# Optimization experiments

Hardware: AMD Instinct MI355X
Metric: run time of the kernel (lower is better)

The kernel has to match this reference:

```python
import jax, jax.numpy as jnp
import numpy as np

N = 50000
E = 400000
IN_DIM = 128
HID = 128
OUT = 128
HEADS = 8
NEG_SLOPE = 0.2  # PyG GATConv default
BN_EPS = 1e-5


def _gat_conv(x, W, a_src, a_dst, b, src, dst, concat):
    """PyG GATConv (eval): self-loops added by caller. x:[N,F], W:[F,H*C], a_*:[H,C]."""
    H, C = a_src.shape
    xW = (x @ W).reshape(N, H, C)                       # [N,H,C]
    es = jnp.sum(xW * a_src[None], axis=-1)             # [N,H]
    ed = jnp.sum(xW * a_dst[None], axis=-1)             # [N,H]
    e = jax.nn.leaky_relu(es[src] + ed[dst], NEG_SLOPE) # [E,H]
    m = jax.ops.segment_max(e, dst, num_segments=N)     # softmax over incoming edges per dst
    ex = jnp.exp(e - m[dst])
    denom = jax.ops.segment_sum(ex, dst, num_segments=N)
    alpha = ex / denom[dst]                             # [E,H]
    out = jax.ops.segment_sum(xW[src] * alpha[:, :, None], dst, num_segments=N)  # [N,H,C]
    out = out.reshape(N, H * C) if concat else out.mean(axis=1)
    return out + b


def _bn_eval(h, g, be, rm, rv):
    return (h - rm) * jax.lax.rsqrt(rv + BN_EPS) * g + be


def setup_inputs() -> dict:
    key = jax.random.key(0)
    ks = jax.random.split(key, 20)
    C1 = HID // HEADS
    f32 = jnp.float32
    inp = {
        "x": jax.random.normal(ks[0], (N, IN_DIM), dtype=f32),
        "edge_index": jax.random.randint(ks[1], (2, E), 0, N, dtype=jnp.int64),
        # GAT layer 1 (in->hid, 8 heads, concat)
        "W1": jax.random.normal(ks[2], (IN_DIM, HEADS * C1), dtype=f32) * 0.05,
        "a_src1": jax.random.normal(ks[3], (HEADS, C1), dtype=f32) * 0.05,
        "a_dst1": jax.random.normal(ks[4], (HEADS, C1), dtype=f32) * 0.05,
        "b1": jnp.zeros((HEADS * C1,), dtype=f32),
        # GAT layer 2 (hid->hid, 8 heads, concat)
        "W2": jax.random.normal(ks[5], (HID, HEADS * C1), dtype=f32) * 0.05,
        "a_src2": jax.random.normal(ks[6], (HEADS, C1), dtype=f32) * 0.05,
        "a_dst2": jax.random.normal(ks[7], (HEADS, C1), dtype=f32) * 0.05,
        "b2": jnp.zeros((HEADS * C1,), dtype=f32),
        # GAT layer 3 (hid->out, 1 head, no concat)
        "W3": jax.random.normal(ks[8], (HID, OUT), dtype=f32) * 0.05,
        "a_src3": jax.random.normal(ks[9], (1, OUT), dtype=f32) * 0.05,
        "a_dst3": jax.random.normal(ks[10], (1, OUT), dtype=f32) * 0.05,
        "b3": jnp.zeros((OUT,), dtype=f32),
        # residual linears
        "R1w": jax.random.normal(ks[11], (IN_DIM, HID), dtype=f32) * 0.05,
        "R1b": jnp.zeros((HID,), dtype=f32),
        "R2w": jax.random.normal(ks[12], (HID, HID), dtype=f32) * 0.05,
        "R2b": jnp.zeros((HID,), dtype=f32),
        "R3w": jax.random.normal(ks[13], (HID, OUT), dtype=f32) * 0.05,
        "R3b": jnp.zeros((OUT,), dtype=f32),
        # batch norms (eval mode: running stats)
        "g1": jnp.ones((HID,), dtype=f32), "be1": jnp.zeros((HID,), dtype=f32),
        "rm1": jnp.zeros((HID,), dtype=f32), "rv1": jnp.ones((HID,), dtype=f32),
        "g2": jnp.ones((HID,), dtype=f32), "be2": jnp.zeros((HID,), dtype=f32),
        "rm2": jnp.zeros((HID,), dtype=f32), "rv2": jnp.ones((HID,), dtype=f32),
    }
    return inp


def reference(x, edge_index, W1, a_src1, a_dst1, b1, W2, a_src2, a_dst2, b2,
              W3, a_src3, a_dst3, b3, R1w, R1b, R2w, R2b, R3w, R3b,
              g1, be1, rm1, rv1, g2, be2, rm2, rv2):
    # PyG GATConv adds self-loops by default
    loops = jnp.arange(N, dtype=edge_index.dtype)
    src = jnp.concatenate([edge_index[0], loops])
    dst = jnp.concatenate([edge_index[1], loops])

    h = _gat_conv(x, W1, a_src1, a_dst1, b1, src, dst, concat=True) + (x @ R1w + R1b)
    h1 = jax.nn.relu(_bn_eval(h, g1, be1, rm1, rv1))  # dropout identity in eval

    h = _gat_conv(h1, W2, a_src2, a_dst2, b2, src, dst, concat=True) + (h1 @ R2w + R2b)
    h2 = jax.nn.relu(_bn_eval(h, g2, be2, rm2, rv2))

    out = _gat_conv(h2, W3, a_src3, a_dst3, b3, src, dst, concat=False) + (h2 @ R3w + R3b)
    return out
```

## Files before the change

### kernel.cpp

```cpp
#include <hip/hip_runtime.h>
#include <hip/hip_bf16.h>
#include <type_traits>

typedef __hip_bfloat16 bf16;
typedef __hip_bfloat162 bf162;
typedef short v8s __attribute__((ext_vector_type(8)));
typedef float v4f __attribute__((ext_vector_type(4)));

__device__ __forceinline__ float lrelu(float x) { return x > 0.f ? x : 0.2f * x; }
__device__ __forceinline__ float b2f(bf16 v) { return __bfloat162float(v); }

__global__ void k_count(const int* __restrict__ ei, int* __restrict__ cnt, int E) {
    int i = blockIdx.x * 256 + threadIdx.x;
    if (i < E) atomicAdd(&cnt[ei[E + i]], 1);
}

__global__ void k_scan1(const int* __restrict__ cnt, int* __restrict__ ofs,
                        int* __restrict__ bsum, int n) {
    __shared__ int sh[256];
    int t = threadIdx.x;
    int base = blockIdx.x * 1024 + t * 4;
    int v[4]; int s = 0;
#pragma unroll
    for (int i = 0; i < 4; ++i) { v[i] = (base + i < n) ? cnt[base + i] : 0; s += v[i]; }
    sh[t] = s; __syncthreads();
    for (int o = 1; o < 256; o <<= 1) {
        int x = 0; if (t >= o) x = sh[t - o];
        __syncthreads();
        sh[t] += x;
        __syncthreads();
    }
    int excl = sh[t] - s;
#pragma unroll
    for (int i = 0; i < 4; ++i) { if (base + i < n) ofs[base + i] = excl; excl += v[i]; }
    if (t == 255) bsum[blockIdx.x] = sh[255];
}

__global__ void k_scan2(const int* __restrict__ bsum, int* __restrict__ bpre, int nb) {
    int l = threadIdx.x;
    int v = (l < nb) ? bsum[l] : 0;
    int orig = v;
    for (int o = 1; o < 64; o <<= 1) {
        int x = __shfl_up(v, o);
        if (l >= o) v += x;
    }
    if (l < nb) bpre[l] = v - orig;
}

__global__ void k_scan3(int* __restrict__ ofs, int* __restrict__ cur,
                        const int* __restrict__ bpre, int n) {
    int i = blockIdx.x * 256 + threadIdx.x;
    if (i < n) { int v = ofs[i] + bpre[i >> 10]; ofs[i] = v; cur[i] = v; }
}

__global__ void k_fill(const int* __restrict__ ei, int* __restrict__ cur,
                       int* __restrict__ csr, int E) {
    int i = blockIdx.x * 256 + threadIdx.x;
    if (i < E) {
        int d = ei[E + i];
        int pos = atomicAdd(&cur[d], 1);
        csr[pos] = ei[i];
    }
}

__global__ void k_trans(const float* __restrict__ s0, const float* __restrict__ s1,
                        const float* __restrict__ s2, const float* __restrict__ s3,
                        const float* __restrict__ s4, const float* __restrict__ s5,
                        const float* __restrict__ as1, const float* __restrict__ ad1,
                        const float* __restrict__ as2, const float* __restrict__ ad2,
                        const float* __restrict__ as3, const float* __restrict__ ad3,
                        const float* b1, const float* R1b, const float* g1, const float* be1,
                        const float* rm1, const float* rv1,
                        const float* b2, const float* R2b, const float* g2, const float* be2,
                        const float* rm2, const float* rv2,
                        const float* b3, const float* R3b,
                        bf16* __restrict__ wt, float* __restrict__ prm) {
    int b = blockIdx.x;
    int t = threadIdx.x;
    if (b == 6) {
        int c = t;
        if (c < 128) {
            float s1v = g1[c] * rsqrtf(rv1[c] + 1e-5f);
            prm[c]       = b1[c] + R1b[c];
            prm[128 + c] = s1v;
            prm[256 + c] = be1[c] - rm1[c] * s1v;
            float s2v = g2[c] * rsqrtf(rv2[c] + 1e-5f);
            prm[384 + c] = b2[c] + R2b[c];
            prm[512 + c] = s2v;
            prm[640 + c] = be2[c] - rm2[c] * s2v;
            prm[768 + c] = b3[c] + R3b[c];
        }
        return;
    }
    const float* src;
    switch (b) {
        case 0: src = s0; break; case 1: src = s1; break; case 2: src = s2; break;
        case 3: src = s3; break; case 4: src = s4; break; default: src = s5; break;
    }
    bf16* dst = wt + (size_t)b * 18432;
    for (int i = t; i < 16384; i += 256) {
        int k = i >> 7, n = i & 127;
        dst[n * 128 + k] = __float2bfloat16(src[i]);
    }
    if ((b & 1) == 0) {
        int layer = b >> 1;
        if (layer < 2) {
            const float* asr = (layer == 0) ? as1 : as2;
            const float* ads = (layer == 0) ? ad1 : ad2;
            for (int i = t; i < 2048; i += 256) {
                int row = i >> 7, k = i & 127, h = row & 7;
                const float* av = (row < 8) ? asr : ads;
                float s = 0.f;
#pragma unroll
                for (int c = 0; c < 16; ++c) s += src[k * 128 + h * 16 + c] * av[h * 16 + c];
                dst[(128 + row) * 128 + k] = __float2bfloat16(s);
            }
        } else {
            for (int i = t; i < 2048; i += 256) {
                int row = i >> 7, k = i & 127;
                float s = 0.f;
                if (row == 0 || row == 8) {
                    const float* av = (row == 0) ? as3 : ad3;
                    for (int c = 0; c < 128; ++c) s += src[k * 128 + c] * av[c];
                }
                dst[(128 + row) * 128 + k] = __float2bfloat16(s);
            }
        }
    } else {
        for (int i = t; i < 2048; i += 256)
            dst[16384 + i] = __float2bfloat16(0.f);
    }
}

template <typename T>
__global__ void gemm_dual(const T* __restrict__ A,
                          const bf16* __restrict__ BT0, const bf16* __restrict__ BT1,
                          bf16* __restrict__ O0, bf16* __restrict__ O1,
                          float* __restrict__ es, float* __restrict__ ed,
                          int mode, int nrows) {
    __shared__ bf16 Ash[128 * 128];
    __shared__ bf16 Bsh[144 * 128];
    const bf16* BT = (blockIdx.y == 0) ? BT0 : BT1;
    bf16* O = (blockIdx.y == 0) ? O0 : O1;
    const int t = threadIdx.x;
    const int rowbase = blockIdx.x * 128;
    {
        const int r = t >> 1, hf = t & 1;
        int gr = rowbase + r; if (gr >= nrows) gr = nrows - 1;
        if constexpr (std::is_same<T, float>::value) {
            const float4* asrc = (const float4*)(A + (size_t)gr * 128 + hf * 64);
#pragma unroll
            for (int j = 0; j < 8; ++j) {
                float4 u = asrc[2 * j], w = asrc[2 * j + 1];
                union { bf16 h[8]; float4 f; } tmp;
                tmp.h[0] = __float2bfloat16(u.x); tmp.h[1] = __float2bfloat16(u.y);
                tmp.h[2] = __float2bfloat16(u.z); tmp.h[3] = __float2bfloat16(u.w);
                tmp.h[4] = __float2bfloat16(w.x); tmp.h[5] = __float2bfloat16(w.y);
                tmp.h[6] = __float2bfloat16(w.z); tmp.h[7] = __float2bfloat16(w.w);
                int c = hf * 8 + j, cp = c ^ (r & 7);
                *(float4*)(&Ash[r * 128 + cp * 8]) = tmp.f;
            }
        } else {
            const float4* asrc = (const float4*)(A + (size_t)gr * 128 + hf * 64);
#pragma unroll
            for (int j = 0; j < 8; ++j) {
                int c = hf * 8 + j, cp = c ^ (r & 7);
                *(float4*)(&Ash[r * 128 + cp * 8]) = asrc[j];
            }
        }
    }
    for (int s = t; s < 288; s += 256) {
        int r = s >> 1, hf = s & 1;
        const float4* bsrc = (const float4*)(BT + r * 128 + hf * 64);
#pragma unroll
        for (int j = 0; j < 8; ++j) {
            int c = hf * 8 + j, cp = c ^ (r & 7);
            *(float4*)(&Bsh[r * 128 + cp * 8]) = bsrc[j];
        }
    }
    __syncthreads();
    const int wave = t >> 6, lane = t & 63, quad = lane >> 4, l16 = lane & 15;
    v4f acc[2][9];
#pragma unroll
    for (int i = 0; i < 2; ++i)
#pragma unroll
        for (int j = 0; j < 9; ++j) acc[i][j] = (v4f){0.f, 0.f, 0.f, 0.f};
#pragma unroll
    for (int kit = 0; kit < 4; ++kit) {
        v8s afr[2], bfr[9];
#pragma unroll
        for (int rt = 0; rt < 2; ++rt) {
            int row = wave * 32 + rt * 16 + l16;
            int cp = (kit * 4 + quad) ^ (row & 7);
            afr[rt] = *(const v8s*)(&Ash[row * 128 + cp * 8]);
        }
#pragma unroll
        for (int ct = 0; ct < 9; ++ct) {
            int nn = ct * 16 + l16;
            int cp = (kit * 4 + quad) ^ (nn & 7);
            bfr[ct] = *(const v8s*)(&Bsh[nn * 128 + cp * 8]);
        }
#pragma unroll
        for (int rt = 0; rt < 2; ++rt)
#pragma unroll
            for (int ct = 0; ct < 9; ++ct)
                acc[rt][ct] = __builtin_amdgcn_mfma_f32_16x16x32_bf16(afr[rt], bfr[ct], acc[rt][ct], 0, 0, 0);
    }
#pragma unroll
    for (int rt = 0; rt < 2; ++rt)
#pragma unroll
        for (int ct = 0; ct < 8; ++ct)
#pragma unroll
            for (int r = 0; r < 4; ++r) {
                int gr = rowbase + wave * 32 + rt * 16 + quad * 4 + r;
                if (gr < nrows) O[(size_t)gr * 128 + ct * 16 + l16] = __float2bfloat16(acc[rt][ct][r]);
            }
    if (mode != 0 && blockIdx.y == 0) {
#pragma unroll
        for (int rt = 0; rt < 2; ++rt)
#pragma unroll
            for (int r = 0; r < 4; ++r) {
                int gr = rowbase + wave * 32 + rt * 16 + quad * 4 + r;
                if (gr < nrows) {
                    float v = acc[rt][8][r];
                    if (mode == 1) {
                        if (l16 < 8) es[(size_t)gr * 8 + l16] = v;
                        else         ed[(size_t)gr * 8 + (l16 - 8)] = v;
                    } else {
                        if (l16 == 0) es[gr] = v;
                        else if (l16 == 8) ed[gr] = v;
                    }
                }
            }
    }
}

__global__ void k_agg8(const bf16* __restrict__ xW, const float* __restrict__ es8,
                       const float* __restrict__ ed8,
                       const int* __restrict__ ofs, const int* __restrict__ cur,
                       const int* __restrict__ csr,
                       const bf16* __restrict__ rres, const float* __restrict__ prm,
                       bf16* __restrict__ hout, int n) {
    int wave = threadIdx.x >> 6, lane = threadIdx.x & 63;
    int node = blockIdx.x * 4 + wave;
    if (node >= n) return;
    const int g = lane >> 4, l16 = lane & 15;
    const int c0 = l16 * 8;
    const int hc = l16 >> 1;
    const int he = lane & 7;
    float edw = ed8[(size_t)node * 8 + he];
    float wselfh = __expf(lrelu(es8[(size_t)node * 8 + he] + edw));
    float acc[8]; float den = 0.f;
#pragma unroll
    for (int i = 0; i < 8; ++i) acc[i] = 0.f;
    {
        float ws = __shfl(wselfh, hc);
        if (g == 0) {
            v8s xv = *(const v8s*)(xW + (size_t)node * 128 + c0);
            const bf16* xb = (const bf16*)&xv;
            den = ws;
#pragma unroll
            for (int i = 0; i < 8; ++i) acc[i] = ws * b2f(xb[i]);
        }
    }
    int beg = ofs[node], end = cur[node];
    for (int base = beg; base < end; base += 64) {
        int m = end - base; if (m > 64) m = 64;
        int idx = (lane < m) ? csr[base + lane] : node;
        for (int sub = 0; sub * 8 < m; ++sub) {
            int e = sub * 8 + (lane >> 3);
            int sidx = __shfl(idx, e & 63);
            float esv = es8[(size_t)sidx * 8 + he];
            float w = (e < m) ? __expf(lrelu(esv + edw)) : 0.f;
#pragma unroll
            for (int jj = 0; jj < 2; ++jj) {
                int jo = jj * 4 + g;
                int j = sub * 8 + jo;
                int sv = __shfl(idx, j & 63);
                float wj = __shfl(w, jo * 8 + hc);
                v8s xv = *(const v8s*)(xW + (size_t)sv * 128 + c0);
                const bf16* xb = (const bf16*)&xv;
                den += wj;
#pragma unroll
                for (int i = 0; i < 8; ++i) acc[i] += wj * b2f(xb[i]);
            }
        }
    }
    den += __shfl_xor(den, 16); den += __shfl_xor(den, 32);
#pragma unroll
    for (int i = 0; i < 8; ++i) {
        acc[i] += __shfl_xor(acc[i], 16);
        acc[i] += __shfl_xor(acc[i], 32);
    }
    if (g == 0) {
        float inv = 1.f / den;
        v8s rv = *(const v8s*)(rres + (size_t)node * 128 + c0);
        const bf16* rb = (const bf16*)&rv;
        bf16 outv[8];
#pragma unroll
        for (int i = 0; i < 8; ++i) {
            int c = c0 + i;
            float v = acc[i] * inv + prm[c] + b2f(rb[i]);
            v = fmaxf(v * prm[128 + c] + prm[256 + c], 0.f);
            outv[i] = __float2bfloat16(v);
        }
        *(v8s*)(hout + (size_t)node * 128 + c0) = *(v8s*)outv;
    }
}

__global__ void k_agg1(const bf16* __restrict__ xW, const float* __restrict__ es,
                       const float* __restrict__ ed,
                       const int* __restrict__ ofs, const int* __restrict__ cur,
                       const int* __restrict__ csr,
                       const bf16* __restrict__ rres, const float* __restrict__ bias,
                       float* __restrict__ out, int n) {
    int wave = threadIdx.x >> 6, lane = threadIdx.x & 63;
    int node = blockIdx.x * 4 + wave;
    if (node >= n) return;
    const int g = lane >> 4, l16 = lane & 15;
    const int c0 = l16 * 8;
    float edv = ed[node];
    float wself = __expf(lrelu(es[node] + edv));
    float acc[8]; float den = 0.f;
#pragma unroll
    for (int i = 0; i < 8; ++i) acc[i] = 0.f;
    if (g == 0) {
        v8s xv = *(const v8s*)(xW + (size_t)node * 128 + c0);
        const bf16* xb = (const bf16*)&xv;
        den = wself;
#pragma unroll
        for (int i = 0; i < 8; ++i) acc[i] = wself * b2f(xb[i]);
    }
    int beg = ofs[node], end = cur[node];
    for (int base = beg; base < end; base += 64) {
        int m = end - base; if (m > 64) m = 64;
        int idx = (lane < m) ? csr[base + lane] : node;
        float w = (lane < m) ? __expf(lrelu(es[idx] + edv)) : 0.f;
        for (int j = 0; j < m; j += 4) {
            int jl = j + g;
            int sv = __shfl(idx, jl & 63);
            float wj = __shfl(w, jl & 63);
            if (jl >= m) wj = 0.f;
            v8s xv = *(const v8s*)(xW + (size_t)sv * 128 + c0);
            const bf16* xb = (const bf16*)&xv;
            den += wj;
#pragma unroll
            for (int i = 0; i < 8; ++i) acc[i] += wj * b2f(xb[i]);
        }
    }
    den += __shfl_xor(den, 16); den += __shfl_xor(den, 32);
#pragma unroll
    for (int i = 0; i < 8; ++i) {
        acc[i] += __shfl_xor(acc[i], 16);
        acc[i] += __shfl_xor(acc[i], 32);
    }
    if (g == 0) {
        float inv = 1.f / den;
        v8s rv = *(const v8s*)(rres + (size_t)node * 128 + c0);
        const bf16* rb = (const bf16*)&rv;
        float ov[8];
#pragma unroll
        for (int i = 0; i < 8; ++i)
            ov[i] = acc[i] * inv + bias[c0 + i] + b2f(rb[i]);
        float4 o0, o1;
        o0.x = ov[0]; o0.y = ov[1]; o0.z = ov[2]; o0.w = ov[3];
        o1.x = ov[4]; o1.y = ov[5]; o1.z = ov[6]; o1.w = ov[7];
        *(float4*)(out + (size_t)node * 128 + c0) = o0;
        *(float4*)(out + (size_t)node * 128 + c0 + 4) = o1;
    }
}

extern "C" void kernel_launch(void* const* d_in, const int* in_sizes, int n_in,
                              void* d_out, int out_size, void* d_ws, size_t ws_size,
                              hipStream_t stream) {
    const float* x   = (const float*)d_in[0];
    const int*   ei  = (const int*)d_in[1];
    const float* W1  = (const float*)d_in[2];
    const float* as1 = (const float*)d_in[3];
    const float* ad1 = (const float*)d_in[4];
    const float* b1  = (const float*)d_in[5];
    const float* W2  = (const float*)d_in[6];
    const float* as2 = (const float*)d_in[7];
    const float* ad2 = (const float*)d_in[8];
    const float* b2  = (const float*)d_in[9];
    const float* W3  = (const float*)d_in[10];
    const float* as3 = (const float*)d_in[11];
    const float* ad3 = (const float*)d_in[12];
    const float* b3  = (const float*)d_in[13];
    const float* R1w = (const float*)d_in[14];
    const float* R1b = (const float*)d_in[15];
    const float* R2w = (const float*)d_in[16];
    const float* R2b = (const float*)d_in[17];
    const float* R3w = (const float*)d_in[18];
    const float* R3b = (const float*)d_in[19];
    const float* g1  = (const float*)d_in[20];
    const float* be1 = (const float*)d_in[21];
    const float* rm1 = (const float*)d_in[22];
    const float* rv1 = (const float*)d_in[23];
    const float* g2  = (const float*)d_in[24];
    const float* be2 = (const float*)d_in[25];
    const float* rm2 = (const float*)d_in[26];
    const float* rv2 = (const float*)d_in[27];

    const int N = in_sizes[0] / 128;
    const int E = in_sizes[1] / 2;

    char* p = (char*)d_ws;
    size_t off = 0;
    auto alloc = [&](size_t b) { void* r = p + off; off = (off + b + 255) & ~(size_t)255; return r; };
    int*   cnt  = (int*)alloc((size_t)N * 4);
    int*   ofs  = (int*)alloc((size_t)N * 4);
    int*   cur  = (int*)alloc((size_t)N * 4);
    int*   bsum = (int*)alloc(64 * 4);
    int*   bpre = (int*)alloc(64 * 4);
    int*   csr  = (int*)alloc((size_t)E * 4);
    bf16*  WT   = (bf16*)alloc((size_t)6 * 18432 * 2);
    float* prm  = (float*)alloc(896 * 4);
    float* es   = (float*)alloc((size_t)N * 8 * 4);
    float* ed   = (float*)alloc((size_t)N * 8 * 4);
    bf16*  xW   = (bf16*)alloc((size_t)N * 128 * 2);
    bf16*  rres = (bf16*)alloc((size_t)N * 128 * 2);
    bf16*  hA   = (bf16*)alloc((size_t)N * 128 * 2);
    bf16*  hB   = (bf16*)alloc((size_t)N * 128 * 2);
    (void)ws_size; (void)n_in; (void)out_size;

    hipMemsetAsync(cnt, 0, (size_t)N * 4, stream);
    const int eb = (E + 255) / 256;
    const int nb = (N + 1023) / 1024;
    k_count<<<eb, 256, 0, stream>>>(ei, cnt, E);
    k_scan1<<<nb, 256, 0, stream>>>(cnt, ofs, bsum, N);
    k_scan2<<<1, 64, 0, stream>>>(bsum, bpre, nb);
    k_scan3<<<(N + 255) / 256, 256, 0, stream>>>(ofs, cur, bpre, N);
    k_fill<<<eb, 256, 0, stream>>>(ei, cur, csr, E);
    k_trans<<<7, 256, 0, stream>>>(W1, R1w, W2, R2w, W3, R3w,
                                   as1, ad1, as2, ad2, as3, ad3,
                                   b1, R1b, g1, be1, rm1, rv1,
                                   b2, R2b, g2, be2, rm2, rv2, b3, R3b,
                                   WT, prm);

    const int gx = (N + 127) / 128;
    const int nw = (N + 3) / 4;
    gemm_dual<float><<<dim3(gx, 2), 256, 0, stream>>>(x, WT, WT + 18432, xW, rres, es, ed, 1, N);
    k_agg8<<<nw, 256, 0, stream>>>(xW, es, ed, ofs, cur, csr, rres, prm, hA, N);
    gemm_dual<bf16><<<dim3(gx, 2), 256, 0, stream>>>(hA, WT + 2 * 18432, WT + 3 * 18432, xW, rres, es, ed, 1, N);
    k_agg8<<<nw, 256, 0, stream>>>(xW, es, ed, ofs, cur, csr, rres, prm + 384, hB, N);
    gemm_dual<bf16><<<dim3(gx, 2), 256, 0, stream>>>(hB, WT + 4 * 18432, WT + 5 * 18432, xW, rres, es, ed, 2, N);
    k_agg1<<<nw, 256, 0, stream>>>(xW, es, ed, ofs, cur, csr, rres, prm + 768, (float*)d_out, N);
}
```

Baseline: 346.7 us.

## Merge CSR build into fewer launches and overlap fill with first GEMM

```diff
diff --git a/kernel.cpp b/kernel.cpp
--- a/kernel.cpp
+++ b/kernel.cpp
@@ -10,73 +10,26 @@
 __device__ __forceinline__ float lrelu(float x) { return x > 0.f ? x : 0.2f * x; }
 __device__ __forceinline__ float b2f(bf16 v) { return __bfloat162float(v); }
 
-__global__ void k_count(const int* __restrict__ ei, int* __restrict__ cnt, int E) {
-    int i = blockIdx.x * 256 + threadIdx.x;
-    if (i < E) atomicAdd(&cnt[ei[E + i]], 1);
-}
-
-__global__ void k_scan1(const int* __restrict__ cnt, int* __restrict__ ofs,
-                        int* __restrict__ bsum, int n) {
-    __shared__ int sh[256];
-    int t = threadIdx.x;
-    int base = blockIdx.x * 1024 + t * 4;
-    int v[4]; int s = 0;
-#pragma unroll
-    for (int i = 0; i < 4; ++i) { v[i] = (base + i < n) ? cnt[base + i] : 0; s += v[i]; }
-    sh[t] = s; __syncthreads();
-    for (int o = 1; o < 256; o <<= 1) {
-        int x = 0; if (t >= o) x = sh[t - o];
-        __syncthreads();
-        sh[t] += x;
-        __syncthreads();
-    }
-    int excl = sh[t] - s;
-#pragma unroll
-    for (int i = 0; i < 4; ++i) { if (base + i < n) ofs[base + i] = excl; excl += v[i]; }
-    if (t == 255) bsum[blockIdx.x] = sh[255];
-}
-
-__global__ void k_scan2(const int* __restrict__ bsum, int* __restrict__ bpre, int nb) {
-    int l = threadIdx.x;
-    int v = (l < nb) ? bsum[l] : 0;
-    int orig = v;
-    for (int o = 1; o < 64; o <<= 1) {
-        int x = __shfl_up(v, o);
-        if (l >= o) v += x;
-    }
-    if (l < nb) bpre[l] = v - orig;
-}
-
-__global__ void k_scan3(int* __restrict__ ofs, int* __restrict__ cur,
-                        const int* __restrict__ bpre, int n) {
-    int i = blockIdx.x * 256 + threadIdx.x;
-    if (i < n) { int v = ofs[i] + bpre[i >> 10]; ofs[i] = v; cur[i] = v; }
-}
-
-__global__ void k_fill(const int* __restrict__ ei, int* __restrict__ cur,
-                       int* __restrict__ csr, int E) {
-    int i = blockIdx.x * 256 + threadIdx.x;
-    if (i < E) {
-        int d = ei[E + i];
-        int pos = atomicAdd(&cur[d], 1);
-        csr[pos] = ei[i];
-    }
-}
-
-__global__ void k_trans(const float* __restrict__ s0, const float* __restrict__ s1,
-                        const float* __restrict__ s2, const float* __restrict__ s3,
-                        const float* __restrict__ s4, const float* __restrict__ s5,
-                        const float* __restrict__ as1, const float* __restrict__ ad1,
-                        const float* __restrict__ as2, const float* __restrict__ ad2,
-                        const float* __restrict__ as3, const float* __restrict__ ad3,
-                        const float* b1, const float* R1b, const float* g1, const float* be1,
-                        const float* rm1, const float* rv1,
-                        const float* b2, const float* R2b, const float* g2, const float* be2,
-                        const float* rm2, const float* rv2,
-                        const float* b3, const float* R3b,
-                        bf16* __restrict__ wt, float* __restrict__ prm) {
+__global__ void k_pre(const float* __restrict__ s0, const float* __restrict__ s1,
+                      const float* __restrict__ s2, const float* __restrict__ s3,
+                      const float* __restrict__ s4, const float* __restrict__ s5,
+                      const float* __restrict__ as1, const float* __restrict__ ad1,
+                      const float* __restrict__ as2, const float* __restrict__ ad2,
+                      const float* __restrict__ as3, const float* __restrict__ ad3,
+                      const float* b1, const float* R1b, const float* g1, const float* be1,
+                      const float* rm1, const float* rv1,
+                      const float* b2, const float* R2b, const float* g2, const float* be2,
+                      const float* rm2, const float* rv2,
+                      const float* b3, const float* R3b,
+                      bf16* __restrict__ wt, float* __restrict__ prm,
+                      const int* __restrict__ ei, int* __restrict__ cnt, int E) {
     int b = blockIdx.x;
     int t = threadIdx.x;
+    if (b >= 7) {
+        int i = (b - 7) * 256 + t;
+        if (i < E) atomicAdd(&cnt[ei[E + i]], 1);
+        return;
+    }
     if (b == 6) {
         int c = t;
         if (c < 128) {
@@ -132,18 +85,41 @@
     }
 }
 
+__global__ void k_scan(const int* __restrict__ cnt, int* __restrict__ ofs,
+                       int* __restrict__ cur, int n) {
+    __shared__ int sh[1024];
+    const int t = threadIdx.x;
+    const int C = (n + 1023) >> 10;
+    const int base = t * C;
+    int s = 0;
+    for (int i = 0; i < C; ++i) { int idx = base + i; if (idx < n) s += cnt[idx]; }
+    sh[t] = s; __syncthreads();
+    for (int o = 1; o < 1024; o <<= 1) {
+        int x = (t >= o) ? sh[t - o] : 0;
+        __syncthreads();
+        sh[t] += x;
+        __syncthreads();
+    }
+    int excl = sh[t] - s;
+    for (int i = 0; i < C; ++i) {
+        int idx = base + i;
+        if (idx < n) { int c = cnt[idx]; ofs[idx] = excl; cur[idx] = excl; excl += c; }
+    }
+}
+
 template <typename T>
-__global__ void gemm_dual(const T* __restrict__ A,
-                          const bf16* __restrict__ BT0, const bf16* __restrict__ BT1,
-                          bf16* __restrict__ O0, bf16* __restrict__ O1,
-                          float* __restrict__ es, float* __restrict__ ed,
-                          int mode, int nrows) {
-    __shared__ bf16 Ash[128 * 128];
-    __shared__ bf16 Bsh[144 * 128];
-    const bf16* BT = (blockIdx.y == 0) ? BT0 : BT1;
-    bf16* O = (blockIdx.y == 0) ? O0 : O1;
+__device__ __forceinline__ void gemm_body(const T* __restrict__ A,
+                                          const bf16* __restrict__ BT0, const bf16* __restrict__ BT1,
+                                          bf16* __restrict__ O0, bf16* __restrict__ O1,
+                                          float* __restrict__ es, float* __restrict__ ed,
+                                          int mode, int nrows, int job, int ntiles,
+                                          bf16* Ash, bf16* Bsh) {
+    const int y = (job >= ntiles) ? 1 : 0;
+    const int tile = y ? job - ntiles : job;
+    const bf16* BT = y ? BT1 : BT0;
+    bf16* O = y ? O1 : O0;
     const int t = threadIdx.x;
-    const int rowbase = blockIdx.x * 128;
+    const int rowbase = tile * 128;
     {
         const int r = t >> 1, hf = t & 1;
         int gr = rowbase + r; if (gr >= nrows) gr = nrows - 1;
@@ -215,7 +191,7 @@
                 int gr = rowbase + wave * 32 + rt * 16 + quad * 4 + r;
                 if (gr < nrows) O[(size_t)gr * 128 + ct * 16 + l16] = __float2bfloat16(acc[rt][ct][r]);
             }
-    if (mode != 0 && blockIdx.y == 0) {
+    if (mode != 0 && y == 0) {
 #pragma unroll
         for (int rt = 0; rt < 2; ++rt)
 #pragma unroll
@@ -233,6 +209,38 @@
                 }
             }
     }
+}
+
+__global__ void k_fillgemm(const float* __restrict__ A,
+                           const bf16* __restrict__ BT0, const bf16* __restrict__ BT1,
+                           bf16* __restrict__ O0, bf16* __restrict__ O1,
+                           float* __restrict__ es, float* __restrict__ ed,
+                           int nrows, int ntiles,
+                           const int* __restrict__ ei, int* __restrict__ cur,
+                           int* __restrict__ csr, int E) {
+    __shared__ bf16 Ash[128 * 128];
+    __shared__ bf16 Bsh[144 * 128];
+    const int njobs = 2 * ntiles;
+    if (blockIdx.x < njobs) {
+        gemm_body<float>(A, BT0, BT1, O0, O1, es, ed, 1, nrows, blockIdx.x, ntiles, Ash, Bsh);
+    } else {
+        int i = (blockIdx.x - njobs) * 256 + threadIdx.x;
+        if (i < E) {
+            int d = ei[E + i];
+            int pos = atomicAdd(&cur[d], 1);
+            csr[pos] = ei[i];
+        }
+    }
+}
+
+__global__ void k_gemm(const bf16* __restrict__ A,
+                       const bf16* __restrict__ BT0, const bf16* __restrict__ BT1,
+                       bf16* __restrict__ O0, bf16* __restrict__ O1,
+                       float* __restrict__ es, float* __restrict__ ed,
+                       int mode, int nrows, int ntiles) {
+    __shared__ bf16 Ash[128 * 128];
+    __shared__ bf16 Bsh[144 * 128];
+    gemm_body<bf16>(A, BT0, BT1, O0, O1, es, ed, mode, nrows, blockIdx.x, ntiles, Ash, Bsh);
 }
 
 __global__ void k_agg8(const bf16* __restrict__ xW, const float* __restrict__ es8,
@@ -268,22 +276,22 @@
         int m = end - base; if (m > 64) m = 64;
         int idx = (lane < m) ? csr[base + lane] : node;
         for (int sub = 0; sub * 8 < m; ++sub) {
+            int j0 = sub * 8 + g, j1 = sub * 8 + 4 + g;
+            int sv0 = __shfl(idx, j0);
+            int sv1 = __shfl(idx, j1);
+            v8s xv0 = *(const v8s*)(xW + (size_t)sv0 * 128 + c0);
+            v8s xv1 = *(const v8s*)(xW + (size_t)sv1 * 128 + c0);
             int e = sub * 8 + (lane >> 3);
             int sidx = __shfl(idx, e & 63);
             float esv = es8[(size_t)sidx * 8 + he];
             float w = (e < m) ? __expf(lrelu(esv + edw)) : 0.f;
-#pragma unroll
-            for (int jj = 0; jj < 2; ++jj) {
-                int jo = jj * 4 + g;
-                int j = sub * 8 + jo;
-                int sv = __shfl(idx, j & 63);
-                float wj = __shfl(w, jo * 8 + hc);
-                v8s xv = *(const v8s*)(xW + (size_t)sv * 128 + c0);
-                const bf16* xb = (const bf16*)&xv;
-                den += wj;
-#pragma unroll
-                for (int i = 0; i < 8; ++i) acc[i] += wj * b2f(xb[i]);
-            }
+            float w0 = __shfl(w, (j0 - sub * 8) * 8 + hc);
+            float w1 = __shfl(w, (j1 - sub * 8) * 8 + hc);
+            const bf16* xb0 = (const bf16*)&xv0;
+            const bf16* xb1 = (const bf16*)&xv1;
+            den += w0 + w1;
+#pragma unroll
+            for (int i = 0; i < 8; ++i) acc[i] += w0 * b2f(xb0[i]) + w1 * b2f(xb1[i]);
         }
     }
     den += __shfl_xor(den, 16); den += __shfl_xor(den, 32);
@@ -411,8 +419,6 @@
     int*   cnt  = (int*)alloc((size_t)N * 4);
     int*   ofs  = (int*)alloc((size_t)N * 4);
     int*   cur  = (int*)alloc((size_t)N * 4);
-    int*   bsum = (int*)alloc(64 * 4);
-    int*   bpre = (int*)alloc(64 * 4);
     int*   csr  = (int*)alloc((size_t)E * 4);
     bf16*  WT   = (bf16*)alloc((size_t)6 * 18432 * 2);
     float* prm  = (float*)alloc(896 * 4);
@@ -424,26 +430,22 @@
     bf16*  hB   = (bf16*)alloc((size_t)N * 128 * 2);
     (void)ws_size; (void)n_in; (void)out_size;
 
-    hipMemsetAsync(cnt, 0, (size_t)N * 4, stream);
     const int eb = (E + 255) / 256;
-    const int nb = (N + 1023) / 1024;
-    k_count<<<eb, 256, 0, stream>>>(ei, cnt, E);
-    k_scan1<<<nb, 256, 0, stream>>>(cnt, ofs, bsum, N);
-    k_scan2<<<1, 64, 0, stream>>>(bsum, bpre, nb);
-    k_scan3<<<(N + 255) / 256, 256, 0, stream>>>(ofs, cur, bpre, N);
-    k_fill<<<eb, 256, 0, stream>>>(ei, cur, csr, E);
-    k_trans<<<7, 256, 0, stream>>>(W1, R1w, W2, R2w, W3, R3w,
-                                   as1, ad1, as2, ad2, as3, ad3,
-                                   b1, R1b, g1, be1, rm1, rv1,
-                                   b2, R2b, g2, be2, rm2, rv2, b3, R3b,
-                                   WT, prm);
-
     const int gx = (N + 127) / 128;
     const int nw = (N + 3) / 4;
-    gemm_dual<float><<<dim3(gx, 2), 256, 0, stream>>>(x, WT, WT + 18432, xW, rres, es, ed, 1, N);
+
+    hipMemsetAsync(cnt, 0, (size_t)N * 4, stream);
+    k_pre<<<7 + eb, 256, 0, stream>>>(W1, R1w, W2, R2w, W3, R3w,
+                                      as1, ad1, as2, ad2, as3, ad3,
+                                      b1, R1b, g1, be1, rm1, rv1,
+                                      b2, R2b, g2, be2, rm2, rv2, b3, R3b,
+                                      WT, prm, ei, cnt, E);
+    k_scan<<<1, 1024, 0, stream>>>(cnt, ofs, cur, N);
+    k_fillgemm<<<2 * gx + eb, 256, 0, stream>>>(x, WT, WT + 18432, xW, rres, es, ed,
+                                                N, gx, ei, cur, csr, E);
     k_agg8<<<nw, 256, 0, stream>>>(xW, es, ed, ofs, cur, csr, rres, prm, hA, N);
-    gemm_dual<bf16><<<dim3(gx, 2), 256, 0, stream>>>(hA, WT + 2 * 18432, WT + 3 * 18432, xW, rres, es, ed, 1, N);
+    k_gemm<<<2 * gx, 256, 0, stream>>>(hA, WT + 2 * 18432, WT + 3 * 18432, xW, rres, es, ed, 1, N, gx);
     k_agg8<<<nw, 256, 0, stream>>>(xW, es, ed, ofs, cur, csr, rres, prm + 384, hB, N);
-    gemm_dual<bf16><<<dim3(gx, 2), 256, 0, stream>>>(hB, WT + 4 * 18432, WT + 5 * 18432, xW, rres, es, ed, 2, N);
+    k_gemm<<<2 * gx, 256, 0, stream>>>(hB, WT + 4 * 18432, WT + 5 * 18432, xW, rres, es, ed, 2, N, gx);
     k_agg1<<<nw, 256, 0, stream>>>(xW, es, ed, ofs, cur, csr, rres, prm + 768, (float*)d_out, N);
 }
```

Measured after the change: 445.6 us. 28.5% more time.
